# Performance work log

Hardware: AMD Instinct MI355X
Metric: run time of the kernel (lower is better)

The kernel has to match this reference:

```python
import jax, jax.numpy as jnp
import numpy as np

B, S, D, H = 4, 1024, 1024, 16
HD = D // H


def setup_inputs() -> dict:
    key = jax.random.key(0)
    ks = jax.random.split(key, 8)
    q = jax.random.normal(ks[0], (B, S, D), jnp.float32)
    q_mask = jnp.ones((B, S), dtype=bool)
    kv_mask = jax.random.randint(ks[1], (B, S), 0, 2).astype(bool)
    edge_weights = jax.random.uniform(ks[2], (B, S, S), jnp.float32)
    w_init = 0.02
    wq = jax.random.normal(ks[3], (D, D), jnp.float32) * w_init
    wk = jax.random.normal(ks[4], (D, D), jnp.float32) * w_init
    wv = jax.random.normal(ks[5], (D, D), jnp.float32) * w_init
    wo = jax.random.normal(ks[6], (D, D), jnp.float32) * w_init
    bo = jnp.zeros((D,), jnp.float32)
    return {"q": q, "q_mask": q_mask, "kv_mask": kv_mask,
            "edge_weights": edge_weights, "wq": wq, "wk": wk, "wv": wv,
            "wo": wo, "bo": bo}


def _pass_with_mask(x, w, mask, b=None):
    # Linear applied everywhere, padded rows zeroed (matches pass_with_mask)
    y = x @ w.T
    if b is not None:
        y = y + b
    return jnp.where(mask[..., None], y, 0.0)


def reference(q, q_mask, kv_mask, edge_weights, wq, wk, wv, wo, bo):
    b = q.shape[0]
    # merge_masks: padding mask outer product (recv x send)
    full_mask = (q_mask[:, :, None] & kv_mask[:, None, :])[:, None]  # [b,1,s,s]
    # projections (self attention: k = v = q)
    qh = _pass_with_mask(q, wq, q_mask).reshape(b, S, H, HD).transpose(0, 2, 1, 3)
    kh = _pass_with_mask(q, wk, kv_mask).reshape(b, S, H, HD).transpose(0, 2, 1, 3)
    vh = _pass_with_mask(q, wv, kv_mask).reshape(b, S, H, HD).transpose(0, 2, 1, 3)
    # NOTE: faithful to source, scaled by sqrt(model_dim), not sqrt(head_dim)
    scores = jnp.einsum("bhqd,bhkd->bhqk", qh, kh) / np.sqrt(D).astype(np.float32)
    scores = scores * edge_weights[:, None]          # mul_weights=True
    scores = jnp.where(full_mask, scores, -jnp.inf)
    scores = jax.nn.softmax(scores, axis=-1)
    scores = jnp.where(full_mask, scores, 0.0)       # re-zero masked entries
    out = jnp.einsum("bhqk,bhkd->bhqd", scores, vh)
    out = out.transpose(0, 2, 1, 3).reshape(b, S, D)
    return _pass_with_mask(out, wo, q_mask, bo)
```

## Files before the change

kernel.cpp:

```cpp
#include <hip/hip_runtime.h>

typedef unsigned short u16;
typedef unsigned int u32;
typedef __bf16 b16x8 __attribute__((ext_vector_type(8)));
typedef u16 u16x8 __attribute__((ext_vector_type(8)));
typedef float f32x4 __attribute__((ext_vector_type(4)));
typedef float f32x16 __attribute__((ext_vector_type(16)));
typedef u32 u32x2 __attribute__((ext_vector_type(2)));

#define DEV __device__ __forceinline__
#define INF __builtin_inff()
#define MFMA16(a, b, c) __builtin_amdgcn_mfma_f32_16x16x32_bf16((a), (b), (c), 0, 0, 0)
#define MFMA32(a, b, c) __builtin_amdgcn_mfma_f32_32x32x16_bf16((a), (b), (c), 0, 0, 0)
#define EXP2F(x) __builtin_amdgcn_exp2f(x)

DEV u16 f2b(float f) {
  union { float f; unsigned u; } x; x.f = f;
  unsigned r = x.u + 0x7fffu + ((x.u >> 16) & 1u);
  return (u16)(r >> 16);
}

DEV u32 pk2(float a, float b) {
  __bf16 lo = (__bf16)a, hi = (__bf16)b;
  u16 ul, uh;
  __builtin_memcpy(&ul, &lo, 2);
  __builtin_memcpy(&uh, &hi, 2);
  return (u32)ul | ((u32)uh << 16);
}

DEV float b2f(u16 v) {
  union { u32 u; float f; } x; x.u = (u32)v << 16; return x.f;
}

DEV void gl_lds16(const u16* g, u16* l) {
  __builtin_amdgcn_global_load_lds((const __attribute__((address_space(1))) void*)g,
                                   (__attribute__((address_space(3))) void*)l, 16, 0, 0);
}

__global__ __launch_bounds__(256) void cvt_all(const float* __restrict__ q,
                                               const float* __restrict__ wq,
                                               const float* __restrict__ wk,
                                               const float* __restrict__ wv,
                                               const float* __restrict__ wo,
                                               u16* __restrict__ xb, u16* __restrict__ wqb,
                                               u16* __restrict__ wkb, u16* __restrict__ wvb,
                                               u16* __restrict__ wob) {
  const int blk = blockIdx.x;
  const float* src; u16* dst; float scale = 1.f; int base;
  if (blk < 4096)      { src = q;  dst = xb;  base = blk; }
  else if (blk < 5120) { src = wq; dst = wqb; base = blk - 4096; scale = 0.045084441f; }
  else if (blk < 6144) { src = wk; dst = wkb; base = blk - 5120; }
  else if (blk < 7168) { src = wv; dst = wvb; base = blk - 6144; }
  else                 { src = wo; dst = wob; base = blk - 7168; }
  const int i = base * 256 + threadIdx.x;
  float4 v = reinterpret_cast<const float4*>(src)[i];
  ushort4 o;
  o.x = f2b(v.x * scale);
  o.y = f2b(v.y * scale);
  o.z = f2b(v.z * scale);
  o.w = f2b(v.w * scale);
  reinterpret_cast<ushort4*>(dst)[i] = o;
}

template <int MODE>
DEV void gemm_body(u16* __restrict__ SA, u16* __restrict__ SB, int m0, int n0,
                   const u16* __restrict__ A, const u16* __restrict__ W,
                   u16* __restrict__ Ybf) {
  const int t = threadIdx.x;
  const int lane = t & 63, w = t >> 6;
  const int lr = lane & 15, lg = lane >> 4;
  const int wr = w >> 1, wc = w & 1;

  f32x4 acc[4][4] = {};

  const int r0 = t >> 2;
  const int xw = (r0 >> 1) & 3;
  const int c0 = (((t & 3) ^ xw)) * 8;
  const int xa = (lr >> 1) & 3;
  const u16* gA = A + (size_t)(m0 + r0) * 1024 + c0;
  const u16* gB = W + (size_t)(n0 + r0) * 1024 + c0;

  auto stage = [&](int buf, int kt) {
    const int ko = kt * 32;
    u16* lA = SA + buf * 4096 + w * 512;
    u16* lB = SB + buf * 4096 + w * 512;
    gl_lds16(gA + ko, lA);
    gl_lds16(gA + ko + 64 * 1024, lA + 2048);
    gl_lds16(gB + ko, lB);
    gl_lds16(gB + ko + 64 * 1024, lB + 2048);
  };

  stage(0, 0);
  __syncthreads();
  for (int kt = 0; kt < 32; ++kt) {
    const int cur = kt & 1;
    if (kt < 31) stage(cur ^ 1, kt + 1);
    const u16* As = SA + cur * 4096;
    const u16* Bs = SB + cur * 4096;
    b16x8 af[4], bf[4];
#pragma unroll
    for (int m = 0; m < 4; ++m)
      af[m] = *reinterpret_cast<const b16x8*>(As + (wr * 64 + m * 16 + lr) * 32 + ((lg ^ xa) * 8));
#pragma unroll
    for (int n = 0; n < 4; ++n)
      bf[n] = *reinterpret_cast<const b16x8*>(Bs + (wc * 64 + n * 16 + lr) * 32 + ((lg ^ xa) * 8));
#pragma unroll
    for (int m = 0; m < 4; ++m)
#pragma unroll
      for (int n = 0; n < 4; ++n)
        acc[m][n] = MFMA16(af[m], bf[n], acc[m][n]);
    __syncthreads();
  }

#pragma unroll
  for (int m = 0; m < 4; ++m) {
    const int row = m0 + wr * 64 + m * 16 + lg * 4;
#pragma unroll
    for (int n = 0; n < 4; ++n) {
      const int col = n0 + wc * 64 + n * 16 + lr;
#pragma unroll
      for (int r = 0; r < 4; ++r) {
        const int rowg = row + r;
        const float v = acc[m][n][r];
        if (MODE == 1) {
          const int bb = rowg >> 10, rw = rowg & 1023, rt = rw >> 5, rl = rw & 31;
          const int h = col >> 6, dh = col & 63;
          const int s = dh >> 4, hi = (dh >> 3) & 1, j = dh & 7;
          size_t idx = (((size_t)((bb * 16 + h) * 32 + rt) * 4 + s) * 64 + (rl + (hi << 5))) * 8 + j;
          Ybf[idx] = f2b(v);
        } else {
          const int bb = rowg >> 10, kv = rowg & 1023, kvt = kv >> 5, kvl = kv & 31;
          const int s = kvl >> 4, k16 = kvl & 15;
          const int hi = (k16 >> 2) & 1;
          const int j = (k16 & 3) | (((k16 >> 3) & 1) << 2);
          const int h = col >> 6, dh = col & 63, d = dh >> 5;
          size_t idx = ((((size_t)((bb * 16 + h) * 32 + kvt) * 2 + d) * 2 + s) * 64 + ((dh & 31) + (hi << 5))) * 8 + j;
          Ybf[idx] = f2b(v);
        }
      }
    }
  }
}

__global__ __launch_bounds__(256, 4) void gemm_qkv(const u16* __restrict__ X,
                                                   const u16* __restrict__ Wq,
                                                   const u16* __restrict__ Wk,
                                                   const u16* __restrict__ Wv,
                                                   u16* __restrict__ Yq, u16* __restrict__ Yk,
                                                   u16* __restrict__ Yv,
                                                   const float* __restrict__ edge,
                                                   u16* __restrict__ Ef) {
  __shared__ __attribute__((aligned(16))) u16 SU[4 * 4096];
  const int id = blockIdx.x;
  const int tid = threadIdx.x;
  if (id >= 768) {
    float (*Ls)[132] = reinterpret_cast<float(*)[132]>(SU);
    const int rr = id - 768;
    const int c = rr & 7, qt = (rr >> 3) & 31, b = rr >> 8;
#pragma unroll
    for (int it = 0; it < 4; ++it) {
      int idx = it * 256 + tid;
      int r = idx >> 5, k4 = idx & 31;
      f32x4 v = *reinterpret_cast<const f32x4*>(
          edge + (size_t)(b * 1024 + qt * 32 + r) * 1024 + c * 128 + k4 * 4);
      *reinterpret_cast<f32x4*>(&Ls[r][k4 * 4]) = v;
    }
    __syncthreads();
#pragma unroll
    for (int it = 0; it < 2; ++it) {
      int slot = it * 256 + tid;
      int kvtl = slot >> 7, i = (slot >> 6) & 1, lane = slot & 63;
      int qv = lane & 31, hi = lane >> 5;
      u16x8 o;
#pragma unroll
      for (int jp = 0; jp < 8; ++jp) {
        int j = i * 8 + jp;
        int kvl = (j & 3) + 8 * (j >> 2) + 4 * hi;
        o[jp] = f2b(Ls[qv][kvtl * 32 + kvl]);
      }
      *reinterpret_cast<u16x8*>(
          Ef + ((size_t)(b * 32 + qt) * 32 + (c * 4 + kvtl)) * 1024 + i * 512 + lane * 8) = o;
    }
    return;
  }
  u16* SA = SU;
  u16* SB = SU + 2 * 4096;
  const int swz = (id & 7) * 96 + (id >> 3);
  const int z = swz >> 8, rem = swz & 255;
  const int by = rem >> 3, bx = rem & 7;
  const int m0 = by * 128, n0 = bx * 128;
  if (z == 0)      gemm_body<1>(SA, SB, m0, n0, X, Wq, Yq);
  else if (z == 1) gemm_body<1>(SA, SB, m0, n0, X, Wk, Yk);
  else             gemm_body<2>(SA, SB, m0, n0, X, Wv, Yv);
}

__global__ __launch_bounds__(256, 4) void gemm_final64(const u16* __restrict__ A,
                                                       const u16* __restrict__ Wo,
                                                       float* __restrict__ Out,
                                                       const float* __restrict__ bias,
                                                       const int* __restrict__ qmask) {
  __shared__ __attribute__((aligned(16))) u16 SA[2 * 2048];
  __shared__ __attribute__((aligned(16))) u16 SB[2 * 4096];
  const int id = blockIdx.x;
  const int swz = (id & 7) * 64 + (id >> 3);
  const int by = swz >> 3, bx = swz & 7;
  const int m0 = by * 64, n0 = bx * 128;
  const int t = threadIdx.x;
  const int lane = t & 63, w = t >> 6;
  const int lr = lane & 15, lg = lane >> 4;
  const int wr = w >> 1, wc = w & 1;

  f32x4 acc[2][4] = {};

  const int r0 = t >> 2;
  const int xw = (r0 >> 1) & 3;
  const int c0 = (((t & 3) ^ xw)) * 8;
  const int xa = (lr >> 1) & 3;
  const u16* gA = A + (size_t)(m0 + r0) * 1024 + c0;
  const u16* gB = Wo + (size_t)(n0 + r0) * 1024 + c0;

  auto stage = [&](int buf, int kt) {
    const int ko = kt * 32;
    u16* lA = SA + buf * 2048 + w * 512;
    u16* lB = SB + buf * 4096 + w * 512;
    gl_lds16(gA + ko, lA);
    gl_lds16(gB + ko, lB);
    gl_lds16(gB + ko + 64 * 1024, lB + 2048);
  };

  stage(0, 0);
  __syncthreads();
  for (int kt = 0; kt < 32; ++kt) {
    const int cur = kt & 1;
    if (kt < 31) stage(cur ^ 1, kt + 1);
    const u16* As = SA + cur * 2048;
    const u16* Bs = SB + cur * 4096;
    b16x8 af[2], bf[4];
#pragma unroll
    for (int m = 0; m < 2; ++m)
      af[m] = *reinterpret_cast<const b16x8*>(As + (wr * 32 + m * 16 + lr) * 32 + ((lg ^ xa) * 8));
#pragma unroll
    for (int n = 0; n < 4; ++n)
      bf[n] = *reinterpret_cast<const b16x8*>(Bs + (wc * 64 + n * 16 + lr) * 32 + ((lg ^ xa) * 8));
#pragma unroll
    for (int m = 0; m < 2; ++m)
#pragma unroll
      for (int n = 0; n < 4; ++n)
        acc[m][n] = MFMA16(af[m], bf[n], acc[m][n]);
    __syncthreads();
  }

#pragma unroll
  for (int m = 0; m < 2; ++m) {
    const int row = m0 + wr * 32 + m * 16 + lg * 4;
#pragma unroll
    for (int n = 0; n < 4; ++n) {
      const int col = n0 + wc * 64 + n * 16 + lr;
#pragma unroll
      for (int r = 0; r < 4; ++r) {
        float y = acc[m][n][r] + bias[col];
        Out[(size_t)(row + r) * 1024 + col] = qmask[row + r] ? y : 0.f;
      }
    }
  }
}

__global__ __launch_bounds__(256, 2) void attn_kernel(
    const u16* __restrict__ Qf, const u16* __restrict__ Kf,
    const u16* __restrict__ Vf, const u16* __restrict__ Ef,
    const int* __restrict__ kvm, u16* __restrict__ out) {
  __shared__ float Osh[3][64][33];
  __shared__ float Lsh[4][32];
  __shared__ __attribute__((aligned(16))) u16 Fsh[1024];

  const int d0 = blockIdx.x;
  const int logical = (d0 & 7) * 256 + (d0 >> 3);
  const int qt = logical & 31, bh = logical >> 5;
  const int b = bh >> 4, h = bh & 15;
  const int tid = threadIdx.x, lane = tid & 63, w = tid >> 6;
  const int ql = lane & 31, hi = lane >> 5;
  const int qrow = qt * 32 + ql;

#pragma unroll
  for (int e = 0; e < 4; ++e) {
    int idx = tid * 4 + e;
    int kt = idx >> 5, h2 = (idx >> 4) & 1, j = idx & 15;
    int kv = kt * 32 + 8 * (j >> 2) + 4 * h2 + (j & 3);
    Fsh[idx] = kvm[b * 1024 + kv] ? (u16)0 : (u16)0xFF80;
  }

  const u16* qp = Qf + (size_t)bh * 65536 + qt * 2048 + lane * 8;
  b16x8 Qr[4];
#pragma unroll
  for (int s = 0; s < 4; ++s) Qr[s] = *reinterpret_cast<const b16x8*>(qp + s * 512);

  const u16* kp = Kf + (size_t)bh * 65536 + lane * 8;
  const u16* vp = Vf + (size_t)bh * 65536 + lane * 8;
  const u16* ep = Ef + (size_t)(b * 32 + qt) * 32768 + lane * 8;

  f32x16 O0 = {}, O1 = {};
  float La[4] = {};

  struct KB { b16x8 K[4]; };
  struct EB { u16x8 E[2]; };
  KB Ka, Kb;
  EB E0, E1, E2, E3;

  auto fK = [&](KB& T, int kvt) {
#pragma unroll
    for (int s = 0; s < 4; ++s)
      T.K[s] = *reinterpret_cast<const b16x8*>(kp + kvt * 2048 + s * 512);
  };
  auto fE = [&](EB& T, int kvt) {
#pragma unroll
    for (int i = 0; i < 2; ++i)
      T.E[i] = *reinterpret_cast<const u16x8*>(ep + kvt * 1024 + i * 512);
  };

  auto compute = [&](const KB& K, const EB& E, int kvt) {
    b16x8 V[4];
#pragma unroll
    for (int ds = 0; ds < 4; ++ds)
      V[ds] = *reinterpret_cast<const b16x8*>(vp + kvt * 2048 + ds * 512);
    u16x8 Fm0 = *reinterpret_cast<const u16x8*>(&Fsh[kvt * 32 + hi * 16]);
    u16x8 Fm1 = *reinterpret_cast<const u16x8*>(&Fsh[kvt * 32 + hi * 16 + 8]);
    f32x16 S = {};
#pragma unroll
    for (int s = 0; s < 4; ++s) S = MFMA32(K.K[s], Qr[s], S);
    float p[16];
#pragma unroll
    for (int j = 0; j < 8; ++j)
      p[j] = EXP2F(fmaf(S[j], b2f(E.E[0][j]), b2f(Fm0[j])));
#pragma unroll
    for (int j = 0; j < 8; ++j)
      p[8 + j] = EXP2F(fmaf(S[8 + j], b2f(E.E[1][j]), b2f(Fm1[j])));
#pragma unroll
    for (int j = 0; j < 16; ++j) La[j & 3] += p[j];
#pragma unroll
    for (int s = 0; s < 2; ++s) {
      union { u32 wd[4]; b16x8 v; } U;
      U.wd[0] = pk2(p[8 * s + 0], p[8 * s + 1]);
      U.wd[1] = pk2(p[8 * s + 2], p[8 * s + 3]);
      U.wd[2] = pk2(p[8 * s + 4], p[8 * s + 5]);
      U.wd[3] = pk2(p[8 * s + 6], p[8 * s + 7]);
      O0 = MFMA32(V[s], U.v, O0);
      O1 = MFMA32(V[2 + s], U.v, O1);
    }
  };

  const int base = w * 8;
  fE(E0, base); fE(E1, base + 1); fE(E2, base + 2);
  fK(Ka, base);
  __syncthreads();

  fE(E3, base + 3); fK(Kb, base + 1); compute(Ka, E0, base + 0);
  fE(E0, base + 4); fK(Ka, base + 2); compute(Kb, E1, base + 1);
  fE(E1, base + 5); fK(Kb, base + 3); compute(Ka, E2, base + 2);
  fE(E2, base + 6); fK(Ka, base + 4); compute(Kb, E3, base + 3);
  fE(E3, base + 7); fK(Kb, base + 5); compute(Ka, E0, base + 4);
                    fK(Ka, base + 6); compute(Kb, E1, base + 5);
                    fK(Kb, base + 7); compute(Ka, E2, base + 6);
                                      compute(Kb, E3, base + 7);

  float Lw = (La[0] + La[1]) + (La[2] + La[3]);
  Lw += __shfl_xor(Lw, 32, 64);

  if (hi == 0) Lsh[w][ql] = Lw;
  if (w > 0) {
#pragma unroll
    for (int r = 0; r < 16; ++r) Osh[w - 1][lane][r] = O0[r];
#pragma unroll
    for (int r = 0; r < 16; ++r) Osh[w - 1][lane][16 + r] = O1[r];
  }
  __syncthreads();
  if (w == 0) {
    float Lg = (Lsh[0][ql] + Lsh[1][ql]) + (Lsh[2][ql] + Lsh[3][ql]);
#pragma unroll
    for (int wv = 0; wv < 3; ++wv) {
#pragma unroll
      for (int r = 0; r < 16; ++r) O0[r] += Osh[wv][lane][r];
#pragma unroll
      for (int r = 0; r < 16; ++r) O1[r] += Osh[wv][lane][16 + r];
    }
    const float inv = (Lg > 0.f) ? 1.f / Lg : 0.f;
    u16* orow = out + (size_t)(b * 1024 + qrow) * 1024 + h * 64 + hi * 4;
#pragma unroll
    for (int H = 0; H < 2; ++H) {
#pragma unroll
      for (int g = 0; g < 4; ++g) {
        float o0 = (H ? O1[4 * g + 0] : O0[4 * g + 0]) * inv;
        float o1 = (H ? O1[4 * g + 1] : O0[4 * g + 1]) * inv;
        float o2 = (H ? O1[4 * g + 2] : O0[4 * g + 2]) * inv;
        float o3 = (H ? O1[4 * g + 3] : O0[4 * g + 3]) * inv;
        u32x2 wv2 = {pk2(o0, o1), pk2(o2, o3)};
        *reinterpret_cast<u32x2*>(orow + H * 32 + g * 8) = wv2;
      }
    }
  }
}

extern "C" void kernel_launch(void* const* d_in, const int* in_sizes, int n_in,
                              void* d_out, int out_size, void* d_ws, size_t ws_size,
                              hipStream_t stream) {
  (void)in_sizes; (void)n_in; (void)out_size; (void)ws_size;
  const float* q    = (const float*)d_in[0];
  const int*   qm   = (const int*)d_in[1];
  const int*   kvm  = (const int*)d_in[2];
  const float* edge = (const float*)d_in[3];
  const float* wq   = (const float*)d_in[4];
  const float* wk   = (const float*)d_in[5];
  const float* wv   = (const float*)d_in[6];
  const float* wo   = (const float*)d_in[7];
  const float* bo   = (const float*)d_in[8];
  float* out = (float*)d_out;

  char* ws = (char*)d_ws;
  u16* xb  = (u16*)(ws);
  u16* wqb = (u16*)(ws + (8ull  << 20));
  u16* wkb = (u16*)(ws + (10ull << 20));
  u16* wvb = (u16*)(ws + (12ull << 20));
  u16* wob = (u16*)(ws + (14ull << 20));
  u16* Qfb = (u16*)(ws + (16ull << 20));
  u16* Kf  = (u16*)(ws + (24ull << 20));
  u16* Vf  = (u16*)(ws + (32ull << 20));
  u16* Ef  = (u16*)(ws + (40ull << 20));
  u16* ab  = xb;

  cvt_all<<<8192, 256, 0, stream>>>(q, wq, wk, wv, wo, xb, wqb, wkb, wvb, wob);
  gemm_qkv<<<1792, 256, 0, stream>>>(xb, wqb, wkb, wvb, Qfb, Kf, Vf, edge, Ef);
  attn_kernel<<<2048, 256, 0, stream>>>(Qfb, Kf, Vf, Ef, kvm, ab);
  gemm_final64<<<512, 256, 0, stream>>>(ab, wob, out, bo, qm);
}
```

Measured before the change: 104.5 us.

## Fuse Q/K/V projections into one GEMM sharing the activation tile

Replaces the three separate 128x128 projection tiles with a single block that loads one 64-row activation tile and computes Q, K and V outputs against three weight tiles. Each X tile is read once for all three projections, and the grid drops from 768 to 512 GEMM blocks. In exchange each block holds 96 accumulators and uses more shared memory (the launch bound falls from 4 to 2 waves per SIMD), so occupancy may drop. Fewer, longer blocks also change the tail behaviour of the GEMM grid.

```diff
diff --git a/kernel.cpp b/kernel.cpp
--- a/kernel.cpp
+++ b/kernel.cpp
@@ -62,104 +62,26 @@
   reinterpret_cast<ushort4*>(dst)[i] = o;
 }
 
-template <int MODE>
-DEV void gemm_body(u16* __restrict__ SA, u16* __restrict__ SB, int m0, int n0,
-                   const u16* __restrict__ A, const u16* __restrict__ W,
-                   u16* __restrict__ Ybf) {
+__global__ __launch_bounds__(256, 2) void gemm_qkv3(const u16* __restrict__ X,
+                                                    const u16* __restrict__ Wq,
+                                                    const u16* __restrict__ Wk,
+                                                    const u16* __restrict__ Wv,
+                                                    u16* __restrict__ Yq, u16* __restrict__ Yk,
+                                                    u16* __restrict__ Yv,
+                                                    const float* __restrict__ edge,
+                                                    u16* __restrict__ Ef) {
+  __shared__ __attribute__((aligned(16))) u16 SA[2 * 2048];
+  __shared__ __attribute__((aligned(16))) u16 SB[3][2 * 4096];
+  const int id = blockIdx.x;
   const int t = threadIdx.x;
-  const int lane = t & 63, w = t >> 6;
-  const int lr = lane & 15, lg = lane >> 4;
-  const int wr = w >> 1, wc = w & 1;
-
-  f32x4 acc[4][4] = {};
-
-  const int r0 = t >> 2;
-  const int xw = (r0 >> 1) & 3;
-  const int c0 = (((t & 3) ^ xw)) * 8;
-  const int xa = (lr >> 1) & 3;
-  const u16* gA = A + (size_t)(m0 + r0) * 1024 + c0;
-  const u16* gB = W + (size_t)(n0 + r0) * 1024 + c0;
-
-  auto stage = [&](int buf, int kt) {
-    const int ko = kt * 32;
-    u16* lA = SA + buf * 4096 + w * 512;
-    u16* lB = SB + buf * 4096 + w * 512;
-    gl_lds16(gA + ko, lA);
-    gl_lds16(gA + ko + 64 * 1024, lA + 2048);
-    gl_lds16(gB + ko, lB);
-    gl_lds16(gB + ko + 64 * 1024, lB + 2048);
-  };
-
-  stage(0, 0);
-  __syncthreads();
-  for (int kt = 0; kt < 32; ++kt) {
-    const int cur = kt & 1;
-    if (kt < 31) stage(cur ^ 1, kt + 1);
-    const u16* As = SA + cur * 4096;
-    const u16* Bs = SB + cur * 4096;
-    b16x8 af[4], bf[4];
-#pragma unroll
-    for (int m = 0; m < 4; ++m)
-      af[m] = *reinterpret_cast<const b16x8*>(As + (wr * 64 + m * 16 + lr) * 32 + ((lg ^ xa) * 8));
-#pragma unroll
-    for (int n = 0; n < 4; ++n)
-      bf[n] = *reinterpret_cast<const b16x8*>(Bs + (wc * 64 + n * 16 + lr) * 32 + ((lg ^ xa) * 8));
-#pragma unroll
-    for (int m = 0; m < 4; ++m)
-#pragma unroll
-      for (int n = 0; n < 4; ++n)
-        acc[m][n] = MFMA16(af[m], bf[n], acc[m][n]);
-    __syncthreads();
-  }
-
-#pragma unroll
-  for (int m = 0; m < 4; ++m) {
-    const int row = m0 + wr * 64 + m * 16 + lg * 4;
-#pragma unroll
-    for (int n = 0; n < 4; ++n) {
-      const int col = n0 + wc * 64 + n * 16 + lr;
-#pragma unroll
-      for (int r = 0; r < 4; ++r) {
-        const int rowg = row + r;
-        const float v = acc[m][n][r];
-        if (MODE == 1) {
-          const int bb = rowg >> 10, rw = rowg & 1023, rt = rw >> 5, rl = rw & 31;
-          const int h = col >> 6, dh = col & 63;
-          const int s = dh >> 4, hi = (dh >> 3) & 1, j = dh & 7;
-          size_t idx = (((size_t)((bb * 16 + h) * 32 + rt) * 4 + s) * 64 + (rl + (hi << 5))) * 8 + j;
-          Ybf[idx] = f2b(v);
-        } else {
-          const int bb = rowg >> 10, kv = rowg & 1023, kvt = kv >> 5, kvl = kv & 31;
-          const int s = kvl >> 4, k16 = kvl & 15;
-          const int hi = (k16 >> 2) & 1;
-          const int j = (k16 & 3) | (((k16 >> 3) & 1) << 2);
-          const int h = col >> 6, dh = col & 63, d = dh >> 5;
-          size_t idx = ((((size_t)((bb * 16 + h) * 32 + kvt) * 2 + d) * 2 + s) * 64 + ((dh & 31) + (hi << 5))) * 8 + j;
-          Ybf[idx] = f2b(v);
-        }
-      }
-    }
-  }
-}
-
-__global__ __launch_bounds__(256, 4) void gemm_qkv(const u16* __restrict__ X,
-                                                   const u16* __restrict__ Wq,
-                                                   const u16* __restrict__ Wk,
-                                                   const u16* __restrict__ Wv,
-                                                   u16* __restrict__ Yq, u16* __restrict__ Yk,
-                                                   u16* __restrict__ Yv,
-                                                   const float* __restrict__ edge,
-                                                   u16* __restrict__ Ef) {
-  __shared__ __attribute__((aligned(16))) u16 SU[4 * 4096];
-  const int id = blockIdx.x;
-  const int tid = threadIdx.x;
-  if (id >= 768) {
-    float (*Ls)[132] = reinterpret_cast<float(*)[132]>(SU);
-    const int rr = id - 768;
+
+  if (id >= 512) {
+    float (*Ls)[132] = reinterpret_cast<float(*)[132]>(&SB[0][0]);
+    const int rr = id - 512;
     const int c = rr & 7, qt = (rr >> 3) & 31, b = rr >> 8;
 #pragma unroll
     for (int it = 0; it < 4; ++it) {
-      int idx = it * 256 + tid;
+      int idx = it * 256 + t;
       int r = idx >> 5, k4 = idx & 31;
       f32x4 v = *reinterpret_cast<const f32x4*>(
           edge + (size_t)(b * 1024 + qt * 32 + r) * 1024 + c * 128 + k4 * 4);
@@ -168,7 +90,7 @@
     __syncthreads();
 #pragma unroll
     for (int it = 0; it < 2; ++it) {
-      int slot = it * 256 + tid;
+      int slot = it * 256 + t;
       int kvtl = slot >> 7, i = (slot >> 6) & 1, lane = slot & 63;
       int qv = lane & 31, hi = lane >> 5;
       u16x8 o;
@@ -183,15 +105,97 @@
     }
     return;
   }
-  u16* SA = SU;
-  u16* SB = SU + 2 * 4096;
-  const int swz = (id & 7) * 96 + (id >> 3);
-  const int z = swz >> 8, rem = swz & 255;
-  const int by = rem >> 3, bx = rem & 7;
-  const int m0 = by * 128, n0 = bx * 128;
-  if (z == 0)      gemm_body<1>(SA, SB, m0, n0, X, Wq, Yq);
-  else if (z == 1) gemm_body<1>(SA, SB, m0, n0, X, Wk, Yk);
-  else             gemm_body<2>(SA, SB, m0, n0, X, Wv, Yv);
+
+  const int swz = (id & 7) * 64 + (id >> 3);
+  const int by = swz >> 3, bx = swz & 7;
+  const int m0 = by * 64, n0 = bx * 128;
+  const int lane = t & 63, w = t >> 6;
+  const int lr = lane & 15, lg = lane >> 4;
+  const int wr = w >> 1, wc = w & 1;
+
+  f32x4 acc[3][2][4] = {};
+
+  const int r0 = t >> 2;
+  const int xw = (r0 >> 1) & 3;
+  const int c0 = (((t & 3) ^ xw)) * 8;
+  const int xa = (lr >> 1) & 3;
+  const u16* gA = X + (size_t)(m0 + r0) * 1024 + c0;
+  const u16* gQ = Wq + (size_t)(n0 + r0) * 1024 + c0;
+  const u16* gK = Wk + (size_t)(n0 + r0) * 1024 + c0;
+  const u16* gV = Wv + (size_t)(n0 + r0) * 1024 + c0;
+
+  auto stage = [&](int buf, int kt) {
+    const int ko = kt * 32;
+    gl_lds16(gA + ko, SA + buf * 2048 + w * 512);
+    u16* lq = SB[0] + buf * 4096 + w * 512;
+    u16* lk = SB[1] + buf * 4096 + w * 512;
+    u16* lv = SB[2] + buf * 4096 + w * 512;
+    gl_lds16(gQ + ko, lq);
+    gl_lds16(gQ + ko + 64 * 1024, lq + 2048);
+    gl_lds16(gK + ko, lk);
+    gl_lds16(gK + ko + 64 * 1024, lk + 2048);
+    gl_lds16(gV + ko, lv);
+    gl_lds16(gV + ko + 64 * 1024, lv + 2048);
+  };
+
+  stage(0, 0);
+  __syncthreads();
+  for (int kt = 0; kt < 32; ++kt) {
+    const int cur = kt & 1;
+    if (kt < 31) stage(cur ^ 1, kt + 1);
+    const u16* As = SA + cur * 2048;
+    b16x8 af[2];
+#pragma unroll
+    for (int m = 0; m < 2; ++m)
+      af[m] = *reinterpret_cast<const b16x8*>(As + (wr * 32 + m * 16 + lr) * 32 + ((lg ^ xa) * 8));
+#pragma unroll
+    for (int z = 0; z < 3; ++z) {
+      const u16* Bs = SB[z] + cur * 4096;
+      b16x8 bf[4];
+#pragma unroll
+      for (int n = 0; n < 4; ++n)
+        bf[n] = *reinterpret_cast<const b16x8*>(Bs + (wc * 64 + n * 16 + lr) * 32 + ((lg ^ xa) * 8));
+#pragma unroll
+      for (int m = 0; m < 2; ++m)
+#pragma unroll
+        for (int n = 0; n < 4; ++n)
+          acc[z][m][n] = MFMA16(af[m], bf[n], acc[z][m][n]);
+    }
+    __syncthreads();
+  }
+
+#pragma unroll
+  for (int z = 0; z < 3; ++z) {
+    u16* Y = (z == 0) ? Yq : (z == 1) ? Yk : Yv;
+#pragma unroll
+    for (int m = 0; m < 2; ++m) {
+      const int row = m0 + wr * 32 + m * 16 + lg * 4;
+#pragma unroll
+      for (int n = 0; n < 4; ++n) {
+        const int col = n0 + wc * 64 + n * 16 + lr;
+#pragma unroll
+        for (int r = 0; r < 4; ++r) {
+          const int rowg = row + r;
+          const float v = acc[z][m][n][r];
+          if (z < 2) {
+            const int bb = rowg >> 10, rw = rowg & 1023, rt = rw >> 5, rl = rw & 31;
+            const int h = col >> 6, dh = col & 63;
+            const int s = dh >> 4, hi = (dh >> 3) & 1, j = dh & 7;
+            size_t idx = (((size_t)((bb * 16 + h) * 32 + rt) * 4 + s) * 64 + (rl + (hi << 5))) * 8 + j;
+            Y[idx] = f2b(v);
+          } else {
+            const int bb = rowg >> 10, kv = rowg & 1023, kvt = kv >> 5, kvl = kv & 31;
+            const int s = kvl >> 4, k16 = kvl & 15;
+            const int hi = (k16 >> 2) & 1;
+            const int j = (k16 & 3) | (((k16 >> 3) & 1) << 2);
+            const int h = col >> 6, dh = col & 63, d = dh >> 5;
+            size_t idx = ((((size_t)((bb * 16 + h) * 32 + kvt) * 2 + d) * 2 + s) * 64 + ((dh & 31) + (hi << 5))) * 8 + j;
+            Y[idx] = f2b(v);
+          }
+        }
+      }
+    }
+  }
 }
 
 __global__ __launch_bounds__(256, 4) void gemm_final64(const u16* __restrict__ A,
@@ -427,7 +431,7 @@
   u16* ab  = xb;
 
   cvt_all<<<8192, 256, 0, stream>>>(q, wq, wk, wv, wo, xb, wqb, wkb, wvb, wob);
-  gemm_qkv<<<1792, 256, 0, stream>>>(xb, wqb, wkb, wvb, Qfb, Kf, Vf, edge, Ef);
+  gemm_qkv3<<<1536, 256, 0, stream>>>(xb, wqb, wkb, wvb, Qfb, Kf, Vf, edge, Ef);
   attn_kernel<<<2048, 256, 0, stream>>>(Qfb, Kf, Vf, Ef, kvm, ab);
   gemm_final64<<<512, 256, 0, stream>>>(ab, wob, out, bo, qm);
 }
```

After: 113.1 us. 1.08x slower.
